# Optimization experiments

Measured on AMD Instinct MI355X. Metric: run time of the kernel, lower is better.

The kernel has to match this reference:

```python
import jax, jax.numpy as jnp
import numpy as np

S, B, D, H = 2048, 2, 256, 8
DK = D // H
EPS = 1e-6
NEG = -1.0e9


def setup_inputs() -> dict:
    key = jax.random.key(0)
    ks = jax.random.split(key, 10)
    s = 1.0 / np.sqrt(D)
    return {
        "q": jax.random.normal(ks[0], (S, B, D), jnp.float32),
        "k": jax.random.normal(ks[1], (S, B, D), jnp.float32),
        "v": jax.random.normal(ks[2], (S, B, D), jnp.float32),
        "graph_pos": jax.random.uniform(ks[3], (S, S, H), jnp.float32),
        "mask": jax.random.randint(ks[4], (B, S, S), 0, 2, jnp.int32),
        # linear weights stored [in, out] so y = x @ W (torch Linear W.T)
        "w_q": jax.random.normal(ks[5], (D, D), jnp.float32) * s,
        "w_k": jax.random.normal(ks[6], (D, D), jnp.float32) * s,
        "w_v": jax.random.normal(ks[7], (D, D), jnp.float32) * s,
        "w_fc": jax.random.normal(ks[8], (D, D), jnp.float32) * s,
        "ln_gamma": jnp.ones((D,), jnp.float32),
        "ln_beta": jnp.zeros((D,), jnp.float32),
    }


def _forward(q, k, v, graph_pos, mask, w_q, w_k, w_v, w_fc, ln_gamma, ln_beta):
    # seq-first -> batch-first: [B, S, D]
    qb = jnp.transpose(q, (1, 0, 2))
    kb = jnp.transpose(k, (1, 0, 2))
    vb = jnp.transpose(v, (1, 0, 2))
    residual = qb
    # project and split heads: [B, H, S, dk]
    qh = (qb @ w_q).reshape(B, S, H, DK).transpose(0, 2, 1, 3)
    kh = (kb @ w_k).reshape(B, S, H, DK).transpose(0, 2, 1, 3)
    vh = (vb @ w_v).reshape(B, S, H, DK).transpose(0, 2, 1, 3)
    temp = jnp.asarray(DK, jnp.float32) ** 0.5
    attn = jnp.einsum("bhqd,bhkd->bhqk", qh / temp, kh)
    attn = jnp.where(mask[:, None] == 0, NEG, attn)
    attno = jax.nn.softmax(attn, axis=-1)  # dropout is identity in eval
    # graph_pos [lk, lq, h] -> [1, h, lq, lk], multiply post-softmax
    bias = jnp.transpose(graph_pos, (2, 1, 0))[None]
    out = jnp.einsum("bhqk,bhkd->bhqd", attno * bias, vh)
    out = out.transpose(0, 2, 1, 3).reshape(B, S, D)
    out = out @ w_fc + residual
    mu = out.mean(-1, keepdims=True)
    var = out.var(-1, keepdims=True)
    out = (out - mu) * jax.lax.rsqrt(var + EPS) * ln_gamma + ln_beta
    return jnp.transpose(out, (1, 0, 2)), attno


def reference(q, k, v, graph_pos, mask, w_q, w_k, w_v, w_fc, ln_gamma, ln_beta):
    return _forward(q, k, v, graph_pos, mask, w_q, w_k, w_v, w_fc, ln_gamma, ln_beta)
```

## Files before the change

### kernel.cpp

```cpp
#include <hip/hip_runtime.h>
#include <hip/hip_bf16.h>

#define S_LEN 2048
#define BATCH 2
#define DMODEL 256
#define NHEAD 8
#define DKH 32
#define NTOK (S_LEN * BATCH)
#define OUT0_ELEMS ((size_t)NTOK * DMODEL)
#define SW (S_LEN / 32)

typedef __bf16 bf16_t;
typedef __bf16 bf16x8 __attribute__((ext_vector_type(8)));
typedef __bf16 bf16x4 __attribute__((ext_vector_type(4)));
typedef float f32x4 __attribute__((ext_vector_type(4)));

#define MFMA16(a, b, c) __builtin_amdgcn_mfma_f32_16x16x32_bf16(a, b, c, 0, 0, 0)

#if defined(__has_builtin)
#if __has_builtin(__builtin_amdgcn_exp2f)
#define EXP2(x) __builtin_amdgcn_exp2f(x)
#endif
#endif
#ifndef EXP2
#define EXP2(x) __expf((x) * 0.6931471805599453f)
#endif

__global__ void k_probe(const unsigned short* __restrict__ q, int* __restrict__ flag) {
  int lane = threadIdx.x & 63;
  int good = 0;
#pragma unroll
  for (int j = 0; j < 4; j++) {
    unsigned short u = q[(lane * 4 + j) * 2];
    int e = (u >> 7) & 0xFF;
    if ((u & 0x7FFF) == 0 || (e >= 110 && e <= 135)) good++;
  }
#pragma unroll
  for (int off = 1; off < 64; off <<= 1) good += __shfl_xor(good, off);
  if (threadIdx.x == 0) *flag = (good >= 200) ? 0 : 1;
}

__global__ __launch_bounds__(256) void k_prep(
    const void* __restrict__ qin, const void* __restrict__ kin,
    const void* __restrict__ vin, bf16_t* __restrict__ qc,
    bf16_t* __restrict__ kc, bf16_t* __restrict__ vc,
    const void* __restrict__ w_q, const void* __restrict__ w_k,
    const void* __restrict__ w_v, const void* __restrict__ w_fc,
    bf16_t* __restrict__ wt, const void* __restrict__ gp,
    bf16_t* __restrict__ gpt, void* __restrict__ attno_raw,
    const int* __restrict__ mask, unsigned int* __restrict__ mbits,
    const int* __restrict__ flag, int mode) {
  __shared__ __align__(16) char smem[32768];
  int bid = blockIdx.x, tid = threadIdx.x;
  int is32 = *flag;

  if (bid < 12288) {
    int which = bid >> 12;
    int i = (bid & 4095) * 256 + tid;
    const void* src = (which == 0) ? qin : (which == 1) ? kin : vin;
    bf16_t* dst = (which == 0) ? qc : (which == 1) ? kc : vc;
    if (i < NTOK * DMODEL)
      dst[i] = is32 ? (bf16_t)((const float*)src)[i] : ((const bf16_t*)src)[i];
    return;
  }

  if (bid < 12544) {
    auto tile = (bf16_t(*)[33])smem;
    int b2 = bid - 12288;
    int bz = b2 >> 6, bx = b2 & 7, by = (b2 >> 3) & 7;
    const void* w = (bz == 0) ? w_q : (bz == 1) ? w_k : (bz == 2) ? w_v : w_fc;
    bf16_t* o = wt + (size_t)bz * DMODEL * DMODEL;
    int tx = tid & 31, ty = tid >> 5;
    int x = bx * 32 + tx, y0 = by * 32;
    for (int j = ty; j < 32; j += 8) {
      size_t idx = (size_t)(y0 + j) * DMODEL + x;
      float v = is32 ? ((const float*)w)[idx] : (float)((const bf16_t*)w)[idx];
      tile[j][tx] = (bf16_t)v;
    }
    __syncthreads();
    for (int j = ty; j < 32; j += 8)
      o[(size_t)(bx * 32 + j) * DMODEL + y0 + tx] = tile[tx][j];
    return;
  }

  auto tile = (float(*)[8][32])smem;
  int b3 = bid - 12544;
  int bx = b3 & 63, by = b3 >> 6;
  int k0 = bx * 32, q0 = by * 32;
  int ci = tid & 63, krl = tid >> 6;
#pragma unroll
  for (int p = 0; p < 8; p++) {
    int kr = p * 4 + krl;
    size_t base = ((size_t)(k0 + kr) * S_LEN + q0) * NHEAD + ci * 4;
    f32x4 v;
    if (is32) {
      v = __builtin_nontemporal_load((const f32x4*)((const float*)gp + base));
    } else {
      bf16x4 bv = *(const bf16x4*)((const bf16_t*)gp + base);
      v[0] = (float)bv[0]; v[1] = (float)bv[1];
      v[2] = (float)bv[2]; v[3] = (float)bv[3];
    }
    int qq = ci >> 1, hb = (ci & 1) * 4;
    tile[kr][hb + 0][qq] = v[0];
    tile[kr][hb + 1][qq] = v[1];
    tile[kr][hb + 2][qq] = v[2];
    tile[kr][hb + 3][qq] = v[3];
  }
  __syncthreads();
  int h = tid >> 5, q = tid & 31;
  if (mode == 0) {
    bf16_t* orow = gpt + ((size_t)h * S_LEN + q0 + q) * S_LEN + k0;
#pragma unroll
    for (int j = 0; j < 4; j++) {
      bf16x8 o;
#pragma unroll
      for (int i2 = 0; i2 < 8; i2++) o[i2] = (bf16_t)tile[j * 8 + i2][h][q];
      *(bf16x8*)(orow + j * 8) = o;
    }
  } else {
    size_t ro = ((size_t)h * S_LEN + q0 + q) * S_LEN + k0;
    size_t bs = (size_t)NHEAD * S_LEN * S_LEN;
    if (is32) {
      float* o0 = (float*)attno_raw + OUT0_ELEMS + ro;
#pragma unroll
      for (int j = 0; j < 8; j++) {
        f32x4 o;
#pragma unroll
        for (int i2 = 0; i2 < 4; i2++) o[i2] = tile[j * 4 + i2][h][q];
        *(f32x4*)(o0 + j * 4) = o;
        *(f32x4*)(o0 + bs + j * 4) = o;
      }
    } else {
      bf16_t* o0 = (bf16_t*)attno_raw + OUT0_ELEMS + ro;
#pragma unroll
      for (int j = 0; j < 4; j++) {
        bf16x8 o;
#pragma unroll
        for (int i2 = 0; i2 < 8; i2++) o[i2] = (bf16_t)tile[j * 8 + i2][h][q];
        *(bf16x8*)(o0 + j * 8) = o;
        *(bf16x8*)(o0 + bs + j * 8) = o;
      }
    }
  }
  if (tid < 64) {
    int w = (by * 64 + bx) * 64 + tid;
    const int* src = mask + (size_t)w * 32;
    unsigned int bits = 0;
#pragma unroll
    for (int j = 0; j < 32; j += 4) {
      int4 m = *(const int4*)(src + j);
      if (m.x) bits |= 1u << j;
      if (m.y) bits |= 1u << (j + 1);
      if (m.z) bits |= 1u << (j + 2);
      if (m.w) bits |= 1u << (j + 3);
    }
    mbits[w] = bits;
  }
}

__global__ __launch_bounds__(256) void k_proj(
    const bf16_t* __restrict__ qin, const bf16_t* __restrict__ kin,
    const bf16_t* __restrict__ vin, const bf16_t* __restrict__ wt,
    bf16_t* __restrict__ qhi, bf16_t* __restrict__ qlo,
    bf16_t* __restrict__ khi, bf16_t* __restrict__ klo,
    bf16_t* __restrict__ vt) {
  int mat = blockIdx.z;
  const bf16_t* x = (mat == 0) ? qin : (mat == 1) ? kin : vin;
  const bf16_t* wm = wt + (size_t)mat * DMODEL * DMODEL;
  int t0 = blockIdx.x * 16;
  int lane = threadIdx.x & 63, wave = threadIdx.x >> 6;
  int col = lane & 15, quad = lane >> 4;
  f32x4 acc[4] = {};
  const bf16_t* xrow = x + (size_t)(t0 + col) * DMODEL + quad * 8;
  for (int kk = 0; kk < 8; kk++) {
    bf16x8 a = *(const bf16x8*)(xrow + kk * 32);
#pragma unroll
    for (int nt = 0; nt < 4; nt++) {
      int n0 = wave * 64 + nt * 16;
      bf16x8 bw = *(const bf16x8*)(wm + (size_t)(n0 + col) * DMODEL + kk * 32 + quad * 8);
      acc[nt] = MFMA16(a, bw, acc[nt]);
    }
  }
  const float qscale = 0.2550348612f;
#pragma unroll
  for (int nt = 0; nt < 4; nt++) {
    int n = wave * 64 + nt * 16 + col;
    int h = n >> 5, dk = n & 31;
#pragma unroll
    for (int r = 0; r < 4; r++) {
      int t = t0 + quad * 4 + r;
      int s = t >> 1, bb = t & 1;
      float val = acc[nt][r];
      if (mat == 0) val *= qscale;
      if (mat <= 1) {
        bf16_t hi = (bf16_t)val;
        bf16_t lo = (bf16_t)(val - (float)hi);
        size_t idx = ((size_t)(bb * NHEAD + h) * S_LEN + s) * DKH + dk;
        if (mat == 0) { qhi[idx] = hi; qlo[idx] = lo; }
        else         { khi[idx] = hi; klo[idx] = lo; }
      } else {
        vt[((size_t)(bb * NHEAD + h) * DKH + dk) * S_LEN + s] = (bf16_t)val;
      }
    }
  }
}

template <int BMODE>
__global__ __launch_bounds__(256, 8) void k_attn(
    const bf16_t* __restrict__ qhi, const bf16_t* __restrict__ qlo,
    const bf16_t* __restrict__ khi, const bf16_t* __restrict__ klo,
    const bf16_t* __restrict__ vtg, const bf16_t* __restrict__ gpt,
    const unsigned int* __restrict__ mbits, void* __restrict__ attno_raw,
    float* __restrict__ attn_out, const int* __restrict__ flag) {
  __shared__ __align__(16) bf16_t lds_pb[4][16][72];
  __shared__ float lds_m[4][16];
  __shared__ float lds_l[4][16];

  int is32 = *flag;
  float*  attno_f = (float*)attno_raw + OUT0_ELEMS;
  bf16_t* attno_b = (bf16_t*)attno_raw + OUT0_ELEMS;

  int L = blockIdx.x;
  int j = L >> 3;
  int p = (L & 7) + ((j >> 7) << 3);
  int h = p >> 1, b = p & 1;
  int q0 = (j & 127) * 16;

  int lane = threadIdx.x & 63, wave = threadIdx.x >> 6;
  int col = lane & 15, quad = lane >> 4;
  int kbase = wave * 512;
  size_t head = (size_t)(b * NHEAD + h);
  const bf16_t* Qh = qhi + head * S_LEN * DKH;
  const bf16_t* Ql = qlo + head * S_LEN * DKH;
  const bf16_t* Kh = khi + head * S_LEN * DKH;
  const bf16_t* Kl = klo + head * S_LEN * DKH;
  const bf16_t* Vt = vtg + head * DKH * S_LEN;
  const unsigned int* mrow =
      mbits + ((size_t)b * S_LEN + q0 + col) * SW + (kbase >> 5);
  const bf16_t* gprow = gpt + ((size_t)h * S_LEN + q0 + col) * S_LEN + kbase;
  size_t brow = head * S_LEN * S_LEN + (size_t)(q0 + col) * S_LEN + kbase;

  bf16x8 qhF = *(const bf16x8*)(Qh + (q0 + col) * DKH + quad * 8);
  bf16x8 qlF = *(const bf16x8*)(Ql + (q0 + col) * DKH + quad * 8);

  float m = -3.0e38f, l = 0.f;
#pragma unroll
  for (int t = 0; t < 32; t++) {
    int k0 = kbase + t * 16;
    bf16x8 khF = *(const bf16x8*)(Kh + (size_t)(k0 + col) * DKH + quad * 8);
    bf16x8 klF = *(const bf16x8*)(Kl + (size_t)(k0 + col) * DKH + quad * 8);
    f32x4 sc = {};
    sc = MFMA16(khF, qhF, sc);
    sc = MFMA16(khF, qlF, sc);
    sc = MFMA16(klF, qhF, sc);
    unsigned int mw = mrow[t >> 1];
    int mb = (int)(mw >> ((t & 1) * 16 + quad * 4)) & 0xF;
    float s0 = (mb & 1) ? sc[0] : -1e9f;
    float s1 = (mb & 2) ? sc[1] : -1e9f;
    float s2 = (mb & 4) ? sc[2] : -1e9f;
    float s3 = (mb & 8) ? sc[3] : -1e9f;
    float tm = fmaxf(fmaxf(s0, s1), fmaxf(s2, s3));
    float m2 = fmaxf(m, tm);
    l = l * EXP2(m - m2) + EXP2(s0 - m2) + EXP2(s1 - m2) +
        EXP2(s2 - m2) + EXP2(s3 - m2);
    m = m2;
  }
#pragma unroll
  for (int off = 16; off < 64; off <<= 1) {
    float mo = __shfl_xor(m, off);
    float lo2 = __shfl_xor(l, off);
    float mn = fmaxf(m, mo);
    l = l * EXP2(m - mn) + lo2 * EXP2(mo - mn);
    m = mn;
  }
  if (lane < 16) { lds_m[wave][lane] = m; lds_l[wave][lane] = l; }
  __syncthreads();
  {
    float mg = -3.0e38f;
#pragma unroll
    for (int w = 0; w < 4; w++) mg = fmaxf(mg, lds_m[w][col]);
    float lg = 0.f;
#pragma unroll
    for (int w = 0; w < 4; w++) lg += lds_l[w][col] * EXP2(lds_m[w][col] - mg);
    m = mg;
    l = lg;
  }
  float invl = 1.0f / l;

  f32x4 oacc[2] = {};
  for (int c = 0; c < 8; c++) {
#pragma unroll
    for (int tt = 0; tt < 4; tt++) {
      int k0 = kbase + c * 64 + tt * 16;
      bf16x8 khF = *(const bf16x8*)(Kh + (size_t)(k0 + col) * DKH + quad * 8);
      bf16x8 klF = *(const bf16x8*)(Kl + (size_t)(k0 + col) * DKH + quad * 8);
      f32x4 sc = {};
      sc = MFMA16(khF, qhF, sc);
      sc = MFMA16(khF, qlF, sc);
      sc = MFMA16(klF, qhF, sc);
      unsigned int mw = mrow[c * 2 + (tt >> 1)];
      int mb = (int)(mw >> ((tt & 1) * 16 + quad * 4)) & 0xF;
      float bias[4];
      if (BMODE == 0) {
        bf16x4 b4 = __builtin_nontemporal_load(
            (const bf16x4*)(gprow + c * 64 + tt * 16 + quad * 4));
#pragma unroll
        for (int r = 0; r < 4; r++) bias[r] = (float)b4[r];
      } else {
        if (is32) {
          f32x4 b4 = *(const f32x4*)(attno_f + brow + c * 64 + tt * 16 + quad * 4);
#pragma unroll
          for (int r = 0; r < 4; r++) bias[r] = b4[r];
        } else {
          bf16x4 b4 = *(const bf16x4*)(attno_b + brow + c * 64 + tt * 16 + quad * 4);
#pragma unroll
          for (int r = 0; r < 4; r++) bias[r] = (float)b4[r];
        }
      }
      f32x4 pf32;
      bf16x4 pv, pbv;
#pragma unroll
      for (int r = 0; r < 4; r++) {
        float sv = (mb & (1 << r)) ? sc[r] : -1e9f;
        float pp = EXP2(sv - m) * invl;
        pf32[r] = pp;
        pv[r] = (bf16_t)pp;
        pbv[r] = (bf16_t)(pp * bias[r]);
      }
      size_t sa = brow + c * 64 + tt * 16 + quad * 4;
      if (is32) *(f32x4*)(attno_f + sa) = pf32;
      else      *(bf16x4*)(attno_b + sa) = pv;
      *(bf16x4*)&lds_pb[wave][col][tt * 16 + quad * 4] = pbv;
    }
#pragma unroll
    for (int ks = 0; ks < 2; ks++) {
      bf16x8 pf = *(const bf16x8*)&lds_pb[wave][col][ks * 32 + quad * 8];
#pragma unroll
      for (int dt = 0; dt < 2; dt++) {
        bf16x8 vf = *(const bf16x8*)(Vt + (size_t)(dt * 16 + col) * S_LEN + kbase + c * 64 + ks * 32 + quad * 8);
        oacc[dt] = MFMA16(vf, pf, oacc[dt]);
      }
    }
  }
  {
    float* lo = (float*)&lds_pb[wave][0][0];
#pragma unroll
    for (int dt = 0; dt < 2; dt++)
#pragma unroll
      for (int r = 0; r < 4; r++)
        lo[col * 34 + dt * 16 + quad * 4 + r] = oacc[dt][r];
  }
  __syncthreads();
  if (wave == 0) {
    int t = (q0 + col) * BATCH + b;
#pragma unroll
    for (int dt = 0; dt < 2; dt++) {
      f32x4 vv = {};
#pragma unroll
      for (int w = 0; w < 4; w++) {
        const float* lw = (const float*)&lds_pb[w][0][0];
#pragma unroll
        for (int r2 = 0; r2 < 4; r2++)
          vv[r2] += lw[col * 34 + dt * 16 + quad * 4 + r2];
      }
      *(f32x4*)(attn_out + (size_t)t * DMODEL + h * DKH + dt * 16 + quad * 4) = vv;
    }
  }
}

__global__ __launch_bounds__(256) void k_fc_ln(
    const float* __restrict__ attn_out, const bf16_t* __restrict__ wtfc,
    const bf16_t* __restrict__ qc, const void* __restrict__ gamma,
    const void* __restrict__ beta, void* __restrict__ out0,
    const int* __restrict__ flag) {
  __shared__ float lds_sx[4][16];
  __shared__ float lds_sq[4][16];
  int is32 = *flag;
  int t0 = blockIdx.x * 16;
  int lane = threadIdx.x & 63, wave = threadIdx.x >> 6;
  int col = lane & 15, quad = lane >> 4;
  f32x4 acc[4] = {};
  const float* arow = attn_out + (size_t)(t0 + col) * DMODEL + quad * 8;
  for (int kk = 0; kk < 8; kk++) {
    float4 a0 = *(const float4*)(arow + kk * 32);
    float4 a1 = *(const float4*)(arow + kk * 32 + 4);
    float av[8] = {a0.x, a0.y, a0.z, a0.w, a1.x, a1.y, a1.z, a1.w};
    bf16x8 ahi, alo;
#pragma unroll
    for (int j = 0; j < 8; j++) {
      bf16_t hi = (bf16_t)av[j];
      ahi[j] = hi;
      alo[j] = (bf16_t)(av[j] - (float)hi);
    }
#pragma unroll
    for (int nt = 0; nt < 4; nt++) {
      int n0 = wave * 64 + nt * 16;
      bf16x8 bfr = *(const bf16x8*)(wtfc + (size_t)(n0 + col) * DMODEL + kk * 32 + quad * 8);
      acc[nt] = MFMA16(ahi, bfr, acc[nt]);
      acc[nt] = MFMA16(alo, bfr, acc[nt]);
    }
  }
#pragma unroll
  for (int nt = 0; nt < 4; nt++) {
    int n = wave * 64 + nt * 16 + col;
#pragma unroll
    for (int r = 0; r < 4; r++) {
      int t = t0 + quad * 4 + r;
      acc[nt][r] += (float)qc[(size_t)t * DMODEL + n];
    }
  }
  float sx[4], sq[4];
#pragma unroll
  for (int r = 0; r < 4; r++) {
    float s = 0, s2 = 0;
#pragma unroll
    for (int nt = 0; nt < 4; nt++) { float v = acc[nt][r]; s += v; s2 += v * v; }
    sx[r] = s; sq[r] = s2;
  }
#pragma unroll
  for (int off = 1; off < 16; off <<= 1) {
#pragma unroll
    for (int r = 0; r < 4; r++) {
      sx[r] += __shfl_xor(sx[r], off);
      sq[r] += __shfl_xor(sq[r], off);
    }
  }
  if (col == 0) {
#pragma unroll
    for (int r = 0; r < 4; r++) {
      lds_sx[wave][quad * 4 + r] = sx[r];
      lds_sq[wave][quad * 4 + r] = sq[r];
    }
  }
  __syncthreads();
#pragma unroll
  for (int r = 0; r < 4; r++) {
    int tl = quad * 4 + r;
    float tsx = lds_sx[0][tl] + lds_sx[1][tl] + lds_sx[2][tl] + lds_sx[3][tl];
    float tsq = lds_sq[0][tl] + lds_sq[1][tl] + lds_sq[2][tl] + lds_sq[3][tl];
    float mu = tsx * (1.0f / 256.0f);
    float var = tsq * (1.0f / 256.0f) - mu * mu;
    float rs = rsqrtf(var + 1e-6f);
    int t = t0 + tl;
#pragma unroll
    for (int nt = 0; nt < 4; nt++) {
      int n = wave * 64 + nt * 16 + col;
      float g = is32 ? ((const float*)gamma)[n] : (float)((const bf16_t*)gamma)[n];
      float bt = is32 ? ((const float*)beta)[n] : (float)((const bf16_t*)beta)[n];
      float val = (acc[nt][r] - mu) * rs * g + bt;
      if (is32) ((float*)out0)[(size_t)t * DMODEL + n] = val;
      else      ((bf16_t*)out0)[(size_t)t * DMODEL + n] = (bf16_t)val;
    }
  }
}

extern "C" void kernel_launch(void* const* d_in, const int* in_sizes, int n_in,
                              void* d_out, int out_size, void* d_ws, size_t ws_size,
                              hipStream_t stream) {
  (void)in_sizes; (void)n_in; (void)out_size;
  const void* qin   = d_in[0];
  const void* kin   = d_in[1];
  const void* vin   = d_in[2];
  const void* gp    = d_in[3];
  const int*  mask  = (const int*)d_in[4];
  const void* w_q   = d_in[5];
  const void* w_k   = d_in[6];
  const void* w_v   = d_in[7];
  const void* w_fc  = d_in[8];
  const void* gamma = d_in[9];
  const void* beta  = d_in[10];

  char* ws = (char*)d_ws;
  bf16_t* wt  = (bf16_t*)(ws);
  int* flag = (int*)(ws + (1u << 19));
  bf16_t* qc  = (bf16_t*)(ws + (1u << 20));
  bf16_t* kc  = (bf16_t*)(ws + (3u << 20));
  bf16_t* vc  = (bf16_t*)(ws + (5u << 20));
  bf16_t* qhi = (bf16_t*)(ws + (7u << 20));
  bf16_t* qlo = (bf16_t*)(ws + (9u << 20));
  bf16_t* khi = (bf16_t*)(ws + (11u << 20));
  bf16_t* klo = (bf16_t*)(ws + (13u << 20));
  bf16_t* vt  = (bf16_t*)(ws + (15u << 20));
  float* attn_out = (float*)(ws + (17u << 20));
  unsigned int* mbits = (unsigned int*)(ws + (21u << 20));
  bf16_t* gpt = (bf16_t*)(ws + (22u << 20));

  bool use_ws_gpt = ws_size >= (((size_t)86 << 20) + 64);

  hipLaunchKernelGGL(k_probe, dim3(1), dim3(64), 0, stream,
                     (const unsigned short*)qin, flag);
  hipLaunchKernelGGL(k_prep, dim3(16640), dim3(256), 0, stream,
                     qin, kin, vin, qc, kc, vc, w_q, w_k, w_v, w_fc, wt,
                     gp, gpt, d_out, mask, mbits, flag, use_ws_gpt ? 0 : 1);
  hipLaunchKernelGGL(k_proj, dim3(256, 1, 3), dim3(256), 0, stream,
                     qc, kc, vc, wt, qhi, qlo, khi, klo, vt);
  if (use_ws_gpt) {
    hipLaunchKernelGGL((k_attn<0>), dim3(2048), dim3(256), 0, stream,
                       qhi, qlo, khi, klo, vt, gpt, mbits, d_out, attn_out, flag);
  } else {
    hipLaunchKernelGGL((k_attn<1>), dim3(2048), dim3(256), 0, stream,
                       qhi, qlo, khi, klo, vt, gpt, mbits, d_out, attn_out, flag);
  }
  hipLaunchKernelGGL(k_fc_ln, dim3(256), dim3(256), 0, stream,
                     attn_out, wt + 3 * DMODEL * DMODEL, qc, gamma, beta, d_out, flag);
}
```

Measured before the change: 708.9 us.

## Drop running-max softmax; sum raw exponentials and batch probability stores

```diff
diff --git a/kernel.cpp b/kernel.cpp
--- a/kernel.cpp
+++ b/kernel.cpp
@@ -213,7 +213,6 @@
     const unsigned int* __restrict__ mbits, void* __restrict__ attno_raw,
     float* __restrict__ attn_out, const int* __restrict__ flag) {
   __shared__ __align__(16) bf16_t lds_pb[4][16][72];
-  __shared__ float lds_m[4][16];
   __shared__ float lds_l[4][16];
 
   int is32 = *flag;
@@ -243,7 +242,7 @@
   bf16x8 qhF = *(const bf16x8*)(Qh + (q0 + col) * DKH + quad * 8);
   bf16x8 qlF = *(const bf16x8*)(Ql + (q0 + col) * DKH + quad * 8);
 
-  float m = -3.0e38f, l = 0.f;
+  f32x4 lacc = {};
 #pragma unroll
   for (int t = 0; t < 32; t++) {
     int k0 = kbase + t * 16;
@@ -255,40 +254,23 @@
     sc = MFMA16(klF, qhF, sc);
     unsigned int mw = mrow[t >> 1];
     int mb = (int)(mw >> ((t & 1) * 16 + quad * 4)) & 0xF;
-    float s0 = (mb & 1) ? sc[0] : -1e9f;
-    float s1 = (mb & 2) ? sc[1] : -1e9f;
-    float s2 = (mb & 4) ? sc[2] : -1e9f;
-    float s3 = (mb & 8) ? sc[3] : -1e9f;
-    float tm = fmaxf(fmaxf(s0, s1), fmaxf(s2, s3));
-    float m2 = fmaxf(m, tm);
-    l = l * EXP2(m - m2) + EXP2(s0 - m2) + EXP2(s1 - m2) +
-        EXP2(s2 - m2) + EXP2(s3 - m2);
-    m = m2;
-  }
-#pragma unroll
-  for (int off = 16; off < 64; off <<= 1) {
-    float mo = __shfl_xor(m, off);
-    float lo2 = __shfl_xor(l, off);
-    float mn = fmaxf(m, mo);
-    l = l * EXP2(m - mn) + lo2 * EXP2(mo - mn);
-    m = mn;
-  }
-  if (lane < 16) { lds_m[wave][lane] = m; lds_l[wave][lane] = l; }
+#pragma unroll
+    for (int r = 0; r < 4; r++) {
+      float sv = (mb & (1 << r)) ? sc[r] : -1e9f;
+      lacc[r] += EXP2(sv);
+    }
+  }
+  float l = (lacc[0] + lacc[1]) + (lacc[2] + lacc[3]);
+  l += __shfl_xor(l, 16);
+  l += __shfl_xor(l, 32);
+  if (lane < 16) lds_l[wave][lane] = l;
   __syncthreads();
-  {
-    float mg = -3.0e38f;
-#pragma unroll
-    for (int w = 0; w < 4; w++) mg = fmaxf(mg, lds_m[w][col]);
-    float lg = 0.f;
-#pragma unroll
-    for (int w = 0; w < 4; w++) lg += lds_l[w][col] * EXP2(lds_m[w][col] - mg);
-    m = mg;
-    l = lg;
-  }
+  l = (lds_l[0][col] + lds_l[1][col]) + (lds_l[2][col] + lds_l[3][col]);
   float invl = 1.0f / l;
 
   f32x4 oacc[2] = {};
   for (int c = 0; c < 8; c++) {
+    f32x4 ps[4];
 #pragma unroll
     for (int tt = 0; tt < 4; tt++) {
       int k0 = kbase + c * 64 + tt * 16;
@@ -302,8 +284,7 @@
       int mb = (int)(mw >> ((tt & 1) * 16 + quad * 4)) & 0xF;
       float bias[4];
       if (BMODE == 0) {
-        bf16x4 b4 = __builtin_nontemporal_load(
-            (const bf16x4*)(gprow + c * 64 + tt * 16 + quad * 4));
+        bf16x4 b4 = *(const bf16x4*)(gprow + c * 64 + tt * 16 + quad * 4);
 #pragma unroll
         for (int r = 0; r < 4; r++) bias[r] = (float)b4[r];
       } else {
@@ -317,20 +298,31 @@
           for (int r = 0; r < 4; r++) bias[r] = (float)b4[r];
         }
       }
-      f32x4 pf32;
-      bf16x4 pv, pbv;
+      bf16x4 pbv;
 #pragma unroll
       for (int r = 0; r < 4; r++) {
         float sv = (mb & (1 << r)) ? sc[r] : -1e9f;
-        float pp = EXP2(sv - m) * invl;
-        pf32[r] = pp;
-        pv[r] = (bf16_t)pp;
+        float pp = EXP2(sv) * invl;
+        ps[tt][r] = pp;
         pbv[r] = (bf16_t)(pp * bias[r]);
       }
-      size_t sa = brow + c * 64 + tt * 16 + quad * 4;
-      if (is32) *(f32x4*)(attno_f + sa) = pf32;
-      else      *(bf16x4*)(attno_b + sa) = pv;
       *(bf16x4*)&lds_pb[wave][col][tt * 16 + quad * 4] = pbv;
+    }
+    {
+      size_t sa0 = brow + c * 64 + quad * 4;
+      if (is32) {
+#pragma unroll
+        for (int tt = 0; tt < 4; tt++)
+          *(f32x4*)(attno_f + sa0 + tt * 16) = ps[tt];
+      } else {
+#pragma unroll
+        for (int tt = 0; tt < 4; tt++) {
+          bf16x4 pv;
+#pragma unroll
+          for (int r = 0; r < 4; r++) pv[r] = (bf16_t)ps[tt][r];
+          *(bf16x4*)(attno_b + sa0 + tt * 16) = pv;
+        }
+      }
     }
 #pragma unroll
     for (int ks = 0; ks < 2; ks++) {
```

After: 650.4 us. 1.09x faster.
